# Kernel optimization log

Measured on AMD Instinct MI355X. Metric: run time of the kernel, lower is better.

Reference implementation:

```python
import jax, jax.numpy as jnp
import numpy as np

N_NODES = 50000
N_EDGES = 800000
D_IN = 128
D_OUT = 128
BN_EPS = 1e-5


def setup_inputs() -> dict:
    key = jax.random.key(0)
    ks = jax.random.split(key, 8)
    node_feats = jax.random.normal(ks[0], (N_NODES, D_IN), dtype=jnp.float32)
    src = jax.random.randint(ks[1], (N_EDGES,), 0, N_NODES, dtype=jnp.int32)
    dst = jax.random.randint(ks[2], (N_EDGES,), 0, N_NODES, dtype=jnp.int32)
    # Glorot-ish init for weights
    scale = 1.0 / np.sqrt(D_IN)
    W = jax.random.normal(ks[3], (D_IN, D_OUT), dtype=jnp.float32) * scale
    b = jnp.zeros((D_OUT,), dtype=jnp.float32)
    Wr = jax.random.normal(ks[4], (D_IN, D_OUT), dtype=jnp.float32) * scale
    br = jnp.zeros((D_OUT,), dtype=jnp.float32)
    gamma = jnp.ones((D_OUT,), dtype=jnp.float32)
    beta = jnp.zeros((D_OUT,), dtype=jnp.float32)
    return {"node_feats": node_feats, "src": src, "dst": dst, "W": W, "b": b,
            "Wr": Wr, "br": br, "gamma": gamma, "beta": beta}


def reference(node_feats, src, dst, W, b, Wr, br, gamma, beta):
    N = node_feats.shape[0]
    ones_e = jnp.ones(src.shape[0], dtype=node_feats.dtype)
    # DGL GraphConv norm='both': D_out^{-1/2} on source side, D_in^{-1/2} on dest side
    deg_out = jnp.clip(jax.ops.segment_sum(ones_e, src, num_segments=N), 1.0)
    deg_in = jnp.clip(jax.ops.segment_sum(ones_e, dst, num_segments=N), 1.0)
    h = node_feats * jax.lax.rsqrt(deg_out)[:, None]        # [N, D_in]
    agg = jax.ops.segment_sum(h[src], dst, num_segments=N)  # gather + scatter-add, [N, D_in]
    agg = agg * jax.lax.rsqrt(deg_in)[:, None]
    gcn = jax.nn.relu(agg @ W + b)                           # GraphConv activation=relu
    res = jax.nn.relu(node_feats @ Wr + br)                  # residual branch
    y = gcn + res
    # BatchNorm1d (training mode: biased batch stats)
    mean = jnp.mean(y, axis=0)
    var = jnp.mean(jnp.square(y - mean), axis=0)
    out = (y - mean) * jax.lax.rsqrt(var + BN_EPS) * gamma + beta
    return out
```

## Files before the change

kernel.cpp:

```cpp
#include <hip/hip_runtime.h>

#define N_NODES 50000
#define N_EDGES 800000
#define D 128
#define BN_EPS 1e-5f
#define AGG_BLOCKS 2048
#define SCAN_BLOCKS 196
#define CHUNKS 64
#define EPC (N_EDGES / CHUNKS)
#define HALF_BINS 25600
#define HALF_U32 12800
#define QUART_BINS 12800
#define QUART_U32 6400
#define NB_MERGE 100

typedef short bf16x8 __attribute__((ext_vector_type(8)));
typedef float f32x4  __attribute__((ext_vector_type(4)));
typedef float f32x2  __attribute__((ext_vector_type(2)));
typedef unsigned int u32x4 __attribute__((ext_vector_type(4)));


__device__ __forceinline__ unsigned int pack_rne(float a, float b) {
    unsigned int ua = __float_as_uint(a); ua += 0x7fffu + ((ua >> 16) & 1u);
    unsigned int ub = __float_as_uint(b); ub += 0x7fffu + ((ub >> 16) & 1u);
    return (ua >> 16) | (ub & 0xffff0000u);
}
__device__ __forceinline__ unsigned short pack1_rne(float a) {
    unsigned int ua = __float_as_uint(a); ua += 0x7fffu + ((ua >> 16) & 1u);
    return (unsigned short)(ua >> 16);
}
__device__ __forceinline__ unsigned char pack1_fp8(float a) {
    unsigned int u = __builtin_amdgcn_cvt_pk_fp8_f32(a, a, 0, false);
    return (unsigned char)(u & 0xffu);
}

__global__ __launch_bounds__(256) void hist_kernel(
        const int* __restrict__ dst, const int* __restrict__ src,
        unsigned int* __restrict__ histD, unsigned int* __restrict__ histS,
        const float* __restrict__ W, const float* __restrict__ Wr,
        uint4* __restrict__ pW, uint4* __restrict__ pWr) {
    __shared__ unsigned int h[HALF_U32];
    int tid = threadIdx.x;
    int c = blockIdx.x, r = blockIdx.y;
    if (c >= CHUNKS) {
        if (r != 0 || blockIdx.z != 0) return;
        int t = (c - CHUNKS) * 256 + tid;
        const float* S = (t & 2048) ? Wr : W;
        uint4* Dst     = (t & 2048) ? pWr : pW;
        int e = t & 2047;
        int lane = e & 63, ks = (e >> 6) & 3, ct = e >> 8;
        int n  = ct * 16 + (lane & 15);
        int k0 = ks * 32 + (lane >> 4) * 8;
        float v[8];
        #pragma unroll
        for (int j = 0; j < 8; j++) v[j] = S[(k0 + j) * D + n];
        uint4 rr;
        rr.x = pack_rne(v[0], v[1]); rr.y = pack_rne(v[2], v[3]);
        rr.z = pack_rne(v[4], v[5]); rr.w = pack_rne(v[6], v[7]);
        Dst[e] = rr;
        return;
    }
    const int* keys = blockIdx.z ? src : dst;
    unsigned int* hist = blockIdx.z ? histS : histD;
    for (int j = tid; j < HALF_U32; j += 256) h[j] = 0u;
    __syncthreads();
    int base = c * EPC;
    int lo = r * HALF_BINS;
    for (int i = tid; i < EPC; i += 256) {
        int b = __builtin_nontemporal_load(keys + base + i) - lo;
        if ((unsigned)b < (unsigned)HALF_BINS)
            atomicAdd(&h[b >> 1], 1u << ((b & 1) * 16));
    }
    __syncthreads();
    unsigned int* out = hist + ((size_t)(r * CHUNKS + c)) * HALF_U32;
    for (int j = tid; j < HALF_U32; j += 256) out[j] = h[j];
}

__global__ __launch_bounds__(256) void merge_kernel(
        unsigned int* __restrict__ histD, unsigned int* __restrict__ histS,
        int* __restrict__ cnt_in, int* __restrict__ cnt_out,
        int* __restrict__ row_ptr, int* __restrict__ blk_sum) {
    __shared__ int sh[256];
    int t = threadIdx.x;
    int q = blockIdx.x * 256 + t;
    int r = blockIdx.y;
    unsigned int* hist = blockIdx.z ? histS : histD;
    int* cnt = blockIdx.z ? cnt_out : cnt_in;
    size_t base = (size_t)r * CHUNKS * HALF_U32 + q;
    unsigned int vals[CHUNKS];
    #pragma unroll
    for (int c = 0; c < CHUNKS; c++)
        vals[c] = hist[base + (size_t)c * HALF_U32];
    unsigned int lo = 0, hi = 0;
    #pragma unroll
    for (int c = 0; c < CHUNKS; c++) {
        unsigned int v = vals[c];
        hist[base + (size_t)c * HALF_U32] = lo | (hi << 16);
        lo += v & 0xffffu; hi += v >> 16;
    }
    int n0 = r * HALF_BINS + q * 2;
    cnt[n0]     = (int)lo;
    cnt[n0 + 1] = (int)hi;
    if (blockIdx.z) return;
    int pair = (int)lo + (int)hi;
    sh[t] = pair;
    __syncthreads();
    int inc = pair;
    #pragma unroll
    for (int off = 1; off < 256; off <<= 1) {
        int u = (t >= off) ? sh[t - off] : 0;
        __syncthreads();
        inc += u; sh[t] = inc;
        __syncthreads();
    }
    int excl = inc - pair;
    row_ptr[n0]     = excl;
    row_ptr[n0 + 1] = excl + (int)lo;
    if (t == 255) blk_sum[r * 50 + blockIdx.x] = inc;
}

__global__ __launch_bounds__(256) void scan3_kernel(
        const int* __restrict__ cnt_in, const int* __restrict__ cnt_out,
        const int* __restrict__ blk_sum, int* __restrict__ row_ptr,
        float* __restrict__ rin, float* __restrict__ rout) {
    __shared__ int sh[256];
    int t = threadIdx.x;
    int v = (t < NB_MERGE) ? blk_sum[t] : 0;
    sh[t] = v;
    __syncthreads();
    int inc = v;
    #pragma unroll
    for (int off = 1; off < 256; off <<= 1) {
        int u = (t >= off) ? sh[t - off] : 0;
        __syncthreads();
        inc += u; sh[t] = inc;
        __syncthreads();
    }
    int i = blockIdx.x * 256 + t;
    if (i < N_NODES) {
        int mb = i >> 9;
        int boff = mb ? sh[mb - 1] : 0;
        row_ptr[i] = row_ptr[i] + boff;
        int ci = cnt_in[i], co = cnt_out[i];
        rin[i]  = rsqrtf((float)(ci > 1 ? ci : 1));
        rout[i] = rsqrtf((float)(co > 1 ? co : 1));
    }
    if (blockIdx.x == SCAN_BLOCKS - 1 && t == 0) row_ptr[N_NODES] = N_EDGES;
}

__global__ __launch_bounds__(512) void fill2_kernel(
        const int* __restrict__ src, const int* __restrict__ dst,
        const int* __restrict__ row_ptr, const unsigned int* __restrict__ histP,
        int* __restrict__ csr_src) {
    __shared__ unsigned int h[QUART_U32];
    int tid = threadIdx.x;
    int c = blockIdx.x, s = blockIdx.y;
    int base = c * EPC;
    for (int j = tid; j < QUART_U32; j += 512) h[j] = 0u;
    __syncthreads();
    int lo = s * QUART_BINS;
    int r = s >> 1;
    const unsigned int* pre_c = histP + ((size_t)(r * CHUNKS + c)) * HALF_U32
                                      + (s & 1) * QUART_U32;
    for (int i = tid; i < EPC; i += 512) {
        int d = __builtin_nontemporal_load(dst + base + i);
        int b = d - lo;
        if ((unsigned)b < (unsigned)QUART_BINS) {
            int shft = (b & 1) * 16;
            unsigned int old = atomicAdd(&h[b >> 1], 1u << shft);
            unsigned int rank = (old >> shft) & 0xffffu;
            unsigned int pre = (pre_c[b >> 1] >> shft) & 0xffffu;
            int p = row_ptr[d] + (int)(pre + rank);
            csr_src[p] = __builtin_nontemporal_load(src + base + i);
        }
    }
}

__global__ __launch_bounds__(256) void gemm_mfma(
        const float* __restrict__ x, const uint4* __restrict__ pW,
        const uint4* __restrict__ pWr, const float* __restrict__ br,
        const float* __restrict__ rout, unsigned char* __restrict__ hwb8,
        unsigned short* __restrict__ resb) {
    __shared__ unsigned short xs[64][136];
    int tid = threadIdx.x, wid = tid >> 6, lane = tid & 63;
    int quad = lane >> 4, l15 = lane & 15;
    int r0b = blockIdx.x * 64;
    const float4* xg = (const float4*)(x + (size_t)r0b * D);
    int maxidx = (N_NODES - r0b) * (D / 4);
    #pragma unroll
    for (int i = 0; i < 8; i++) {
        int idx = tid + 256 * i;
        float4 v = (idx < maxidx) ? xg[idx] : make_float4(0.f, 0.f, 0.f, 0.f);
        int row = idx >> 5, c0 = (idx & 31) * 4;
        *(unsigned int*)&xs[row][c0]     = pack_rne(v.x, v.y);
        *(unsigned int*)&xs[row][c0 + 2] = pack_rne(v.z, v.w);
    }
    __syncthreads();
    int wrow0 = wid * 16;
    bf16x8 A[4];
    #pragma unroll
    for (int ks = 0; ks < 4; ks++)
        A[ks] = *(const bf16x8*)&xs[wrow0 + l15][ks * 32 + quad * 8];
    f32x4 accW[8], accR[8];
    #pragma unroll
    for (int ct = 0; ct < 8; ct++) { accW[ct] = (f32x4)0.f; accR[ct] = (f32x4)0.f; }
    #pragma unroll
    for (int ct = 0; ct < 8; ct++) {
        #pragma unroll
        for (int ks = 0; ks < 4; ks++) {
            union { bf16x8 v; uint4 u; } Bw, Br2;
            Bw.u  = pW [(ct * 4 + ks) * 64 + lane];
            Br2.u = pWr[(ct * 4 + ks) * 64 + lane];
            accW[ct] = __builtin_amdgcn_mfma_f32_16x16x32_bf16(A[ks], Bw.v,  accW[ct], 0, 0, 0);
            accR[ct] = __builtin_amdgcn_mfma_f32_16x16x32_bf16(A[ks], Br2.v, accR[ct], 0, 0, 0);
        }
    }
    int r0 = r0b + wrow0;
    float ro[4]; int rowok[4];
    #pragma unroll
    for (int reg = 0; reg < 4; reg++) {
        int row = r0 + quad * 4 + reg;
        rowok[reg] = row < N_NODES;
        ro[reg] = rout[rowok[reg] ? row : N_NODES - 1];
    }
    #pragma unroll
    for (int ct = 0; ct < 8; ct++) {
        int c = ct * 16 + l15;
        float brv = br[c];
        #pragma unroll
        for (int reg = 0; reg < 4; reg++) {
            int row = r0 + quad * 4 + reg;
            if (rowok[reg]) {
                hwb8[(size_t)row * D + c] = pack1_fp8(accW[ct][reg] * ro[reg]);
                resb[(size_t)row * D + c] = pack1_rne(fmaxf(accR[ct][reg] + brv, 0.f));
            }
        }
    }
}

__device__ __forceinline__ float bf_lo(unsigned int v) { return __uint_as_float(v << 16); }
__device__ __forceinline__ float bf_hi(unsigned int v) { return __uint_as_float(v & 0xffff0000u); }

__device__ __forceinline__ void acc8f8(f32x2* a, const uint2 v) {
    a[0] += __builtin_amdgcn_cvt_pk_f32_fp8(v.x, false);
    a[1] += __builtin_amdgcn_cvt_pk_f32_fp8(v.x, true);
    a[2] += __builtin_amdgcn_cvt_pk_f32_fp8(v.y, false);
    a[3] += __builtin_amdgcn_cvt_pk_f32_fp8(v.y, true);
}
__device__ __forceinline__ void acc8f8m(f32x2* a, const uint2 v, float m) {
    f32x2 m2 = {m, m};
    a[0] += m2 * __builtin_amdgcn_cvt_pk_f32_fp8(v.x, false);
    a[1] += m2 * __builtin_amdgcn_cvt_pk_f32_fp8(v.x, true);
    a[2] += m2 * __builtin_amdgcn_cvt_pk_f32_fp8(v.y, false);
    a[3] += m2 * __builtin_amdgcn_cvt_pk_f32_fp8(v.y, true);
}

__device__ __forceinline__ void gather_accum(
        const unsigned char* __restrict__ hwb8, int myidx, int cnt,
        int qg, int ql, f32x2* a) {
    int i = 0;
    for (; i + 16 <= cnt; i += 16) {
        int p0 = __shfl(myidx, i + qg);
        int p1 = __shfl(myidx, i + 4 + qg);
        int p2 = __shfl(myidx, i + 8 + qg);
        int p3 = __shfl(myidx, i + 12 + qg);
        uint2 v0 = *((const uint2*)(hwb8 + (size_t)p0 * 128) + ql);
        uint2 v1 = *((const uint2*)(hwb8 + (size_t)p1 * 128) + ql);
        uint2 v2 = *((const uint2*)(hwb8 + (size_t)p2 * 128) + ql);
        uint2 v3 = *((const uint2*)(hwb8 + (size_t)p3 * 128) + ql);
        acc8f8(a, v0); acc8f8(a, v1); acc8f8(a, v2); acc8f8(a, v3);
    }
    for (; i + 4 <= cnt; i += 4) {
        int p0 = __shfl(myidx, i + qg);
        uint2 v0 = *((const uint2*)(hwb8 + (size_t)p0 * 128) + ql);
        acc8f8(a, v0);
    }
    int t = cnt - i;
    if (t > 0) {
        int j = i + qg; if (j > cnt - 1) j = cnt - 1;
        int p0 = __shfl(myidx, j);
        uint2 v0 = *((const uint2*)(hwb8 + (size_t)p0 * 128) + ql);
        float m = (qg < t) ? 1.f : 0.f;
        acc8f8m(a, v0, m);
    }
}

__global__ __launch_bounds__(256) void agg_kernel(
        const unsigned char* __restrict__ hwb8, const int* __restrict__ row_ptr,
        const int* __restrict__ csr_src, const float* __restrict__ rin,
        const float* __restrict__ bias, const unsigned short* __restrict__ resb,
        unsigned short* __restrict__ yb, float* __restrict__ parts) {
    __shared__ float red[4 * 256];
    int tid = threadIdx.x;
    int lane = tid & 63, wid = tid >> 6;
    int wave = blockIdx.x * 4 + wid;
    int nw = AGG_BLOCKS * 4;
    int qg = lane >> 4;
    int ql = lane & 15;
    float s1[8] = {0,0,0,0,0,0,0,0}, s2[8] = {0,0,0,0,0,0,0,0};
    float4 bv0, bv1;
    if (lane < 16) {
        bv0 = ((const float4*)bias)[2 * lane];
        bv1 = ((const float4*)bias)[2 * lane + 1];
    }
    int n = wave;
    int e0 = 0, e1 = 0, mi = 0;
    u32x4 rv4 = (u32x4)0u;
    float ri = 0.f;
    if (n < N_NODES) {
        e0 = row_ptr[n]; e1 = row_ptr[n + 1];
        ri = rin[n];
        if (lane < 16) rv4 = __builtin_nontemporal_load((const u32x4*)(resb + (size_t)n * D) + lane);
        int c0 = e1 - e0; if (c0 > 64) c0 = 64;
        mi = (lane < c0) ? __builtin_nontemporal_load(csr_src + e0 + lane) : 0;
    }
    while (n < N_NODES) {
        int nn = n + nw;
        int ne0 = 0, ne1 = 0, nmi = 0;
        u32x4 nrv = (u32x4)0u;
        float nri = 0.f;
        if (nn < N_NODES) {
            ne0 = row_ptr[nn]; ne1 = row_ptr[nn + 1];
            nri = rin[nn];
            if (lane < 16) nrv = __builtin_nontemporal_load((const u32x4*)(resb + (size_t)nn * D) + lane);
            int nc = ne1 - ne0; if (nc > 64) nc = 64;
            nmi = (lane < nc) ? __builtin_nontemporal_load(csr_src + ne0 + lane) : 0;
        }
        f32x2 av[4];
        av[0] = (f32x2)0.f; av[1] = (f32x2)0.f; av[2] = (f32x2)0.f; av[3] = (f32x2)0.f;
        {
            int cnt = e1 - e0; if (cnt > 64) cnt = 64;
            gather_accum(hwb8, mi, cnt, qg, ql, av);
        }
        for (int j0 = e0 + 64; j0 < e1; j0 += 64) {
            int cnt = e1 - j0; if (cnt > 64) cnt = 64;
            int mw = (lane < cnt) ? __builtin_nontemporal_load(csr_src + j0 + lane) : 0;
            gather_accum(hwb8, mw, cnt, qg, ql, av);
        }
        float a[8] = { av[0].x, av[0].y, av[1].x, av[1].y, av[2].x, av[2].y, av[3].x, av[3].y };
        #pragma unroll
        for (int k = 0; k < 8; k++) {
            a[k] += __shfl_xor(a[k], 16);
            a[k] += __shfl_xor(a[k], 32);
        }
        if (lane < 16) {
            float o[8];
            o[0] = fmaxf(a[0] * ri + bv0.x, 0.f) + bf_lo(rv4.x);
            o[1] = fmaxf(a[1] * ri + bv0.y, 0.f) + bf_hi(rv4.x);
            o[2] = fmaxf(a[2] * ri + bv0.z, 0.f) + bf_lo(rv4.y);
            o[3] = fmaxf(a[3] * ri + bv0.w, 0.f) + bf_hi(rv4.y);
            o[4] = fmaxf(a[4] * ri + bv1.x, 0.f) + bf_lo(rv4.z);
            o[5] = fmaxf(a[5] * ri + bv1.y, 0.f) + bf_hi(rv4.z);
            o[6] = fmaxf(a[6] * ri + bv1.z, 0.f) + bf_lo(rv4.w);
            o[7] = fmaxf(a[7] * ri + bv1.w, 0.f) + bf_hi(rv4.w);
            uint4 w;
            w.x = pack_rne(o[0], o[1]); w.y = pack_rne(o[2], o[3]);
            w.z = pack_rne(o[4], o[5]); w.w = pack_rne(o[6], o[7]);
            *((uint4*)(yb + (size_t)n * D) + lane) = w;
            #pragma unroll
            for (int k = 0; k < 8; k++) { s1[k] += o[k]; s2[k] += o[k] * o[k]; }
        }
        n = nn; e0 = ne0; e1 = ne1; mi = nmi; rv4 = nrv; ri = nri;
    }
    if (lane < 16) {
        int c0 = lane * 8;
        #pragma unroll
        for (int k = 0; k < 8; k++) {
            red[wid * 256 + c0 + k]       = s1[k];
            red[wid * 256 + 128 + c0 + k] = s2[k];
        }
    }
    __syncthreads();
    if (tid < 256) {
        float v = red[tid] + red[256 + tid] + red[512 + tid] + red[768 + tid];
        parts[(size_t)blockIdx.x * 256 + tid] = v;
    }
}

__global__ __launch_bounds__(256) void bn_fin2(
        const float* __restrict__ parts, const float* __restrict__ gamma,
        const float* __restrict__ beta, float* __restrict__ scsh) {
    __shared__ float rs1[256], rs2[256];
    int c = blockIdx.x, t = threadIdx.x;
    float s1 = 0.f, s2 = 0.f;
    for (int b = t; b < AGG_BLOCKS; b += 256) {
        s1 += parts[(size_t)b * 256 + c];
        s2 += parts[(size_t)b * 256 + 128 + c];
    }
    rs1[t] = s1; rs2[t] = s2;
    __syncthreads();
    for (int off = 128; off > 0; off >>= 1) {
        if (t < off) { rs1[t] += rs1[t + off]; rs2[t] += rs2[t + off]; }
        __syncthreads();
    }
    if (t == 0) {
        const float invN = 1.0f / (float)N_NODES;
        float mean = rs1[0] * invN;
        float var  = rs2[0] * invN - mean * mean;
        float sc = gamma[c] * rsqrtf(var + BN_EPS);
        scsh[c] = sc;
        scsh[128 + c] = beta[c] - mean * sc;
    }
}

__global__ void norm_kernel(const unsigned short* __restrict__ yb,
                            const float* __restrict__ scsh, float* __restrict__ out) {
    int i = blockIdx.x * blockDim.x + threadIdx.x;
    if (i < N_NODES * 16) {
        uint4 v = ((const uint4*)yb)[i];
        int c = (i & 15) * 8;
        f32x4 o0, o1;
        o0[0] = bf_lo(v.x) * scsh[c]     + scsh[128 + c];
        o0[1] = bf_hi(v.x) * scsh[c + 1] + scsh[128 + c + 1];
        o0[2] = bf_lo(v.y) * scsh[c + 2] + scsh[128 + c + 2];
        o0[3] = bf_hi(v.y) * scsh[c + 3] + scsh[128 + c + 3];
        o1[0] = bf_lo(v.z) * scsh[c + 4] + scsh[128 + c + 4];
        o1[1] = bf_hi(v.z) * scsh[c + 5] + scsh[128 + c + 5];
        o1[2] = bf_lo(v.w) * scsh[c + 6] + scsh[128 + c + 6];
        o1[3] = bf_hi(v.w) * scsh[c + 7] + scsh[128 + c + 7];
        f32x4* ov = (f32x4*)out + (size_t)i * 2;
        __builtin_nontemporal_store(o0, ov);
        __builtin_nontemporal_store(o1, ov + 1);
    }
}

extern "C" void kernel_launch(void* const* d_in, const int* in_sizes, int n_in,
                              void* d_out, int out_size, void* d_ws, size_t ws_size,
                              hipStream_t stream) {
    const float* x     = (const float*)d_in[0];
    const int*   src   = (const int*)d_in[1];
    const int*   dst   = (const int*)d_in[2];
    const float* W     = (const float*)d_in[3];
    const float* b     = (const float*)d_in[4];
    const float* Wr    = (const float*)d_in[5];
    const float* br    = (const float*)d_in[6];
    const float* gamma = (const float*)d_in[7];
    const float* beta  = (const float*)d_in[8];
    float* out = (float*)d_out;

    char* ws = (char*)d_ws;
    int*   cnt_in  = (int*)(ws + 0);
    int*   cnt_out = (int*)(ws + 262144);
    int*   row_ptr = (int*)(ws + 524288);
    float* rin     = (float*)(ws + 786432);
    float* rout    = (float*)(ws + 1048576);
    float* scsh    = (float*)(ws + 1310720);
    int*   blk_sum = (int*)(ws + 1312768);
    int*   csr_src = (int*)(ws + 1576960);
    unsigned char*  hwb8 = (unsigned char*)(ws + 4800000);
    unsigned short* resb = (unsigned short*)(ws + 11200000);
    unsigned short* yb   = (unsigned short*)(ws + 24000000);
    float* parts   = (float*)(ws + 36800000);
    uint4* pW      = (uint4*)(ws + 38897152);
    uint4* pWr     = (uint4*)(ws + 38929920);
    unsigned int* histD = (unsigned int*)(ws + 38962688);
    unsigned int* histS = (unsigned int*)(ws + 45516288);

    hist_kernel<<<dim3(CHUNKS + 16, 2, 2), 256, 0, stream>>>(dst, src, histD, histS, W, Wr, pW, pWr);
    merge_kernel<<<dim3(HALF_U32 / 256, 2, 2), 256, 0, stream>>>(histD, histS, cnt_in, cnt_out, row_ptr, blk_sum);
    scan3_kernel<<<SCAN_BLOCKS, 256, 0, stream>>>(cnt_in, cnt_out, blk_sum, row_ptr, rin, rout);
    fill2_kernel<<<dim3(CHUNKS, 4), 512, 0, stream>>>(src, dst, row_ptr, histD, csr_src);
    gemm_mfma<<<(N_NODES + 63) / 64, 256, 0, stream>>>(x, pW, pWr, br, rout, hwb8, resb);
    agg_kernel<<<AGG_BLOCKS, 256, 0, stream>>>(hwb8, row_ptr, csr_src, rin, b, resb, yb, parts);
    bn_fin2<<<128, 256, 0, stream>>>(parts, gamma, beta, scsh);
    norm_kernel<<<(N_NODES * 16 + 255) / 256, 256, 0, stream>>>(yb, scsh, out);
}
```

Before: 228.6 us.

## Eliminate scan kernel by folding block-offset scan and rsqrt into consumers

Removes the separate scan3 kernel. Each block of fill2 and agg now rescans the 100 merge block sums in shared memory and adds the block offset to row_ptr on the fly. Degree rsqrt values are computed inline from the raw counts instead of being read from rin/rout arrays. The source-degree histogram now uses 16 chunks instead of 64 and needs no prefix pass, which shrinks hist and merge work. The cost is a small redundant scan in every fill and agg block, plus extra arithmetic per node.

```diff
diff --git a/kernel.cpp b/kernel.cpp
--- a/kernel.cpp
+++ b/kernel.cpp
@@ -5,9 +5,10 @@
 #define D 128
 #define BN_EPS 1e-5f
 #define AGG_BLOCKS 2048
-#define SCAN_BLOCKS 196
 #define CHUNKS 64
 #define EPC (N_EDGES / CHUNKS)
+#define SCHUNKS 16
+#define SEPC (N_EDGES / SCHUNKS)
 #define HALF_BINS 25600
 #define HALF_U32 12800
 #define QUART_BINS 12800
@@ -33,6 +34,23 @@
     unsigned int u = __builtin_amdgcn_cvt_pk_fp8_f32(a, a, 0, false);
     return (unsigned char)(u & 0xffu);
 }
+
+__device__ __forceinline__ void scan_blksum(const int* __restrict__ blk_sum,
+                                            int* sh, int t) {
+    int v = (t < NB_MERGE) ? blk_sum[t] : 0;
+    if (t < 256) sh[t] = v;
+    __syncthreads();
+    int inc = v;
+    #pragma unroll
+    for (int off = 1; off < 256; off <<= 1) {
+        int u = (t >= off && t < 256) ? sh[t - off] : 0;
+        __syncthreads();
+        inc += u;
+        if (t < 256) sh[t] = inc;
+        __syncthreads();
+    }
+}
+#define BLK_OFF(sh, mb) ((mb) ? (sh)[(mb) - 1] : 0)
 
 __global__ __launch_bounds__(256) void hist_kernel(
         const int* __restrict__ dst, const int* __restrict__ src,
@@ -41,10 +59,10 @@
         uint4* __restrict__ pW, uint4* __restrict__ pWr) {
     __shared__ unsigned int h[HALF_U32];
     int tid = threadIdx.x;
-    int c = blockIdx.x, r = blockIdx.y;
-    if (c >= CHUNKS) {
-        if (r != 0 || blockIdx.z != 0) return;
-        int t = (c - CHUNKS) * 256 + tid;
+    int x = blockIdx.x, r = blockIdx.y;
+    if (x >= CHUNKS + SCHUNKS) {
+        if (r != 0) return;
+        int t = (x - (CHUNKS + SCHUNKS)) * 256 + tid;
         const float* S = (t & 2048) ? Wr : W;
         uint4* Dst     = (t & 2048) ? pWr : pW;
         int e = t & 2047;
@@ -60,20 +78,31 @@
         Dst[e] = rr;
         return;
     }
-    const int* keys = blockIdx.z ? src : dst;
-    unsigned int* hist = blockIdx.z ? histS : histD;
     for (int j = tid; j < HALF_U32; j += 256) h[j] = 0u;
     __syncthreads();
-    int base = c * EPC;
     int lo = r * HALF_BINS;
-    for (int i = tid; i < EPC; i += 256) {
-        int b = __builtin_nontemporal_load(keys + base + i) - lo;
-        if ((unsigned)b < (unsigned)HALF_BINS)
-            atomicAdd(&h[b >> 1], 1u << ((b & 1) * 16));
-    }
-    __syncthreads();
-    unsigned int* out = hist + ((size_t)(r * CHUNKS + c)) * HALF_U32;
-    for (int j = tid; j < HALF_U32; j += 256) out[j] = h[j];
+    if (x < CHUNKS) {
+        int base = x * EPC;
+        for (int i = tid; i < EPC; i += 256) {
+            int b = __builtin_nontemporal_load(dst + base + i) - lo;
+            if ((unsigned)b < (unsigned)HALF_BINS)
+                atomicAdd(&h[b >> 1], 1u << ((b & 1) * 16));
+        }
+        __syncthreads();
+        unsigned int* out = histD + ((size_t)(r * CHUNKS + x)) * HALF_U32;
+        for (int j = tid; j < HALF_U32; j += 256) out[j] = h[j];
+    } else {
+        int sc = x - CHUNKS;
+        int base = sc * SEPC;
+        for (int i = tid; i < SEPC; i += 256) {
+            int b = __builtin_nontemporal_load(src + base + i) - lo;
+            if ((unsigned)b < (unsigned)HALF_BINS)
+                atomicAdd(&h[b >> 1], 1u << ((b & 1) * 16));
+        }
+        __syncthreads();
+        unsigned int* out = histS + ((size_t)(r * SCHUNKS + sc)) * HALF_U32;
+        for (int j = tid; j < HALF_U32; j += 256) out[j] = h[j];
+    }
 }
 
 __global__ __launch_bounds__(256) void merge_kernel(
@@ -82,26 +111,36 @@
         int* __restrict__ row_ptr, int* __restrict__ blk_sum) {
     __shared__ int sh[256];
     int t = threadIdx.x;
-    int q = blockIdx.x * 256 + t;
-    int r = blockIdx.y;
-    unsigned int* hist = blockIdx.z ? histS : histD;
-    int* cnt = blockIdx.z ? cnt_out : cnt_in;
+    int bx = blockIdx.x;
+    int r = bx / 50;
+    int q = (bx % 50) * 256 + t;
+    int n0 = r * HALF_BINS + q * 2;
+    if (blockIdx.y) {
+        size_t base = (size_t)r * SCHUNKS * HALF_U32 + q;
+        unsigned int lo = 0, hi = 0;
+        #pragma unroll
+        for (int c = 0; c < SCHUNKS; c++) {
+            unsigned int v = histS[base + (size_t)c * HALF_U32];
+            lo += v & 0xffffu; hi += v >> 16;
+        }
+        cnt_out[n0]     = (int)lo;
+        cnt_out[n0 + 1] = (int)hi;
+        return;
+    }
     size_t base = (size_t)r * CHUNKS * HALF_U32 + q;
     unsigned int vals[CHUNKS];
     #pragma unroll
     for (int c = 0; c < CHUNKS; c++)
-        vals[c] = hist[base + (size_t)c * HALF_U32];
+        vals[c] = histD[base + (size_t)c * HALF_U32];
     unsigned int lo = 0, hi = 0;
     #pragma unroll
     for (int c = 0; c < CHUNKS; c++) {
         unsigned int v = vals[c];
-        hist[base + (size_t)c * HALF_U32] = lo | (hi << 16);
+        histD[base + (size_t)c * HALF_U32] = lo | (hi << 16);
         lo += v & 0xffffu; hi += v >> 16;
     }
-    int n0 = r * HALF_BINS + q * 2;
-    cnt[n0]     = (int)lo;
-    cnt[n0 + 1] = (int)hi;
-    if (blockIdx.z) return;
+    cnt_in[n0]     = (int)lo;
+    cnt_in[n0 + 1] = (int)hi;
     int pair = (int)lo + (int)hi;
     sh[t] = pair;
     __syncthreads();
@@ -116,44 +155,17 @@
     int excl = inc - pair;
     row_ptr[n0]     = excl;
     row_ptr[n0 + 1] = excl + (int)lo;
-    if (t == 255) blk_sum[r * 50 + blockIdx.x] = inc;
-}
-
-__global__ __launch_bounds__(256) void scan3_kernel(
-        const int* __restrict__ cnt_in, const int* __restrict__ cnt_out,
-        const int* __restrict__ blk_sum, int* __restrict__ row_ptr,
-        float* __restrict__ rin, float* __restrict__ rout) {
-    __shared__ int sh[256];
-    int t = threadIdx.x;
-    int v = (t < NB_MERGE) ? blk_sum[t] : 0;
-    sh[t] = v;
-    __syncthreads();
-    int inc = v;
-    #pragma unroll
-    for (int off = 1; off < 256; off <<= 1) {
-        int u = (t >= off) ? sh[t - off] : 0;
-        __syncthreads();
-        inc += u; sh[t] = inc;
-        __syncthreads();
-    }
-    int i = blockIdx.x * 256 + t;
-    if (i < N_NODES) {
-        int mb = i >> 9;
-        int boff = mb ? sh[mb - 1] : 0;
-        row_ptr[i] = row_ptr[i] + boff;
-        int ci = cnt_in[i], co = cnt_out[i];
-        rin[i]  = rsqrtf((float)(ci > 1 ? ci : 1));
-        rout[i] = rsqrtf((float)(co > 1 ? co : 1));
-    }
-    if (blockIdx.x == SCAN_BLOCKS - 1 && t == 0) row_ptr[N_NODES] = N_EDGES;
+    if (t == 255) blk_sum[bx] = inc;
 }
 
 __global__ __launch_bounds__(512) void fill2_kernel(
         const int* __restrict__ src, const int* __restrict__ dst,
         const int* __restrict__ row_ptr, const unsigned int* __restrict__ histP,
-        int* __restrict__ csr_src) {
+        const int* __restrict__ blk_sum, int* __restrict__ csr_src) {
     __shared__ unsigned int h[QUART_U32];
+    __shared__ int sho[256];
     int tid = threadIdx.x;
+    scan_blksum(blk_sum, sho, tid);
     int c = blockIdx.x, s = blockIdx.y;
     int base = c * EPC;
     for (int j = tid; j < QUART_U32; j += 512) h[j] = 0u;
@@ -170,7 +182,7 @@
             unsigned int old = atomicAdd(&h[b >> 1], 1u << shft);
             unsigned int rank = (old >> shft) & 0xffffu;
             unsigned int pre = (pre_c[b >> 1] >> shft) & 0xffffu;
-            int p = row_ptr[d] + (int)(pre + rank);
+            int p = row_ptr[d] + BLK_OFF(sho, d >> 9) + (int)(pre + rank);
             csr_src[p] = __builtin_nontemporal_load(src + base + i);
         }
     }
@@ -179,7 +191,7 @@
 __global__ __launch_bounds__(256) void gemm_mfma(
         const float* __restrict__ x, const uint4* __restrict__ pW,
         const uint4* __restrict__ pWr, const float* __restrict__ br,
-        const float* __restrict__ rout, unsigned char* __restrict__ hwb8,
+        const unsigned int* __restrict__ cnt_out, unsigned char* __restrict__ hwb8,
         unsigned short* __restrict__ resb) {
     __shared__ unsigned short xs[64][136];
     int tid = threadIdx.x, wid = tid >> 6, lane = tid & 63;
@@ -221,7 +233,8 @@
     for (int reg = 0; reg < 4; reg++) {
         int row = r0 + quad * 4 + reg;
         rowok[reg] = row < N_NODES;
-        ro[reg] = rout[rowok[reg] ? row : N_NODES - 1];
+        int cw = (int)cnt_out[rowok[reg] ? row : N_NODES - 1];
+        ro[reg] = rsqrtf((float)(cw > 1 ? cw : 1));
     }
     #pragma unroll
     for (int ct = 0; ct < 8; ct++) {
@@ -287,11 +300,14 @@
 
 __global__ __launch_bounds__(256) void agg_kernel(
         const unsigned char* __restrict__ hwb8, const int* __restrict__ row_ptr,
-        const int* __restrict__ csr_src, const float* __restrict__ rin,
+        const int* __restrict__ blk_sum, const unsigned int* __restrict__ cnt_in,
+        const int* __restrict__ csr_src,
         const float* __restrict__ bias, const unsigned short* __restrict__ resb,
         unsigned short* __restrict__ yb, float* __restrict__ parts) {
     __shared__ float red[4 * 256];
+    __shared__ int sho[256];
     int tid = threadIdx.x;
+    scan_blksum(blk_sum, sho, tid);
     int lane = tid & 63, wid = tid >> 6;
     int wave = blockIdx.x * 4 + wid;
     int nw = AGG_BLOCKS * 4;
@@ -308,8 +324,10 @@
     u32x4 rv4 = (u32x4)0u;
     float ri = 0.f;
     if (n < N_NODES) {
-        e0 = row_ptr[n]; e1 = row_ptr[n + 1];
-        ri = rin[n];
+        e0 = row_ptr[n] + BLK_OFF(sho, n >> 9);
+        e1 = row_ptr[n + 1] + BLK_OFF(sho, (n + 1) >> 9);
+        int ci = (int)cnt_in[n];
+        ri = rsqrtf((float)(ci > 1 ? ci : 1));
         if (lane < 16) rv4 = __builtin_nontemporal_load((const u32x4*)(resb + (size_t)n * D) + lane);
         int c0 = e1 - e0; if (c0 > 64) c0 = 64;
         mi = (lane < c0) ? __builtin_nontemporal_load(csr_src + e0 + lane) : 0;
@@ -320,8 +338,10 @@
         u32x4 nrv = (u32x4)0u;
         float nri = 0.f;
         if (nn < N_NODES) {
-            ne0 = row_ptr[nn]; ne1 = row_ptr[nn + 1];
-            nri = rin[nn];
+            ne0 = row_ptr[nn] + BLK_OFF(sho, nn >> 9);
+            ne1 = row_ptr[nn + 1] + BLK_OFF(sho, (nn + 1) >> 9);
+            int ci = (int)cnt_in[nn];
+            nri = rsqrtf((float)(ci > 1 ? ci : 1));
             if (lane < 16) nrv = __builtin_nontemporal_load((const u32x4*)(resb + (size_t)nn * D) + lane);
             int nc = ne1 - ne0; if (nc > 64) nc = 64;
             nmi = (lane < nc) ? __builtin_nontemporal_load(csr_src + ne0 + lane) : 0;
@@ -442,8 +462,6 @@
     int*   cnt_in  = (int*)(ws + 0);
     int*   cnt_out = (int*)(ws + 262144);
     int*   row_ptr = (int*)(ws + 524288);
-    float* rin     = (float*)(ws + 786432);
-    float* rout    = (float*)(ws + 1048576);
     float* scsh    = (float*)(ws + 1310720);
     int*   blk_sum = (int*)(ws + 1312768);
     int*   csr_src = (int*)(ws + 1576960);
@@ -456,12 +474,16 @@
     unsigned int* histD = (unsigned int*)(ws + 38962688);
     unsigned int* histS = (unsigned int*)(ws + 45516288);
 
-    hist_kernel<<<dim3(CHUNKS + 16, 2, 2), 256, 0, stream>>>(dst, src, histD, histS, W, Wr, pW, pWr);
-    merge_kernel<<<dim3(HALF_U32 / 256, 2, 2), 256, 0, stream>>>(histD, histS, cnt_in, cnt_out, row_ptr, blk_sum);
-    scan3_kernel<<<SCAN_BLOCKS, 256, 0, stream>>>(cnt_in, cnt_out, blk_sum, row_ptr, rin, rout);
-    fill2_kernel<<<dim3(CHUNKS, 4), 512, 0, stream>>>(src, dst, row_ptr, histD, csr_src);
-    gemm_mfma<<<(N_NODES + 63) / 64, 256, 0, stream>>>(x, pW, pWr, br, rout, hwb8, resb);
-    agg_kernel<<<AGG_BLOCKS, 256, 0, stream>>>(hwb8, row_ptr, csr_src, rin, b, resb, yb, parts);
+    hist_kernel<<<dim3(CHUNKS + SCHUNKS + 16, 2), 256, 0, stream>>>(
+        dst, src, histD, histS, W, Wr, pW, pWr);
+    merge_kernel<<<dim3(NB_MERGE, 2), 256, 0, stream>>>(
+        histD, histS, (int*)cnt_in, (int*)cnt_out, row_ptr, blk_sum);
+    fill2_kernel<<<dim3(CHUNKS, 4), 512, 0, stream>>>(
+        src, dst, row_ptr, histD, blk_sum, csr_src);
+    gemm_mfma<<<(N_NODES + 63) / 64, 256, 0, stream>>>(
+        x, pW, pWr, br, (const unsigned int*)cnt_out, hwb8, resb);
+    agg_kernel<<<AGG_BLOCKS, 256, 0, stream>>>(
+        hwb8, row_ptr, blk_sum, (const unsigned int*)cnt_in, csr_src, b, resb, yb, parts);
     bn_fin2<<<128, 256, 0, stream>>>(parts, gamma, beta, scsh);
     norm_kernel<<<(N_NODES * 16 + 255) / 256, 256, 0, stream>>>(yb, scsh, out);
 }
```

After: 294.2 us. 28.7% more time.
